# Kernel tuning notes

Hardware: AMD Instinct MI355X
Metric: run time of the kernel (lower is better)

The kernel has to match this reference:

```python
import jax, jax.numpy as jnp
import numpy as np

# --- static config (mirrors init_kwargs) ---
D_MODEL = 512; N_HEADS = 8; E_LAYERS = 2
GLOBAL_TOPK = 32; DOWN_LAYERS = 3; LAYER_NUM = 1
NB = DOWN_LAYERS - LAYER_NUM + 1           # local_band_count = 3
LOCAL_TOPK = GLOBAL_TOPK // NB + 1         # 11
TOPK = GLOBAL_TOPK + NB * LOCAL_TOPK       # all_topk = 65
B, C, L = 16, 32, D_MODEL
LN_EPS = 1e-5


def _layernorm(x, g, b):
    mu = jnp.mean(x, -1, keepdims=True)
    var = jnp.mean((x - mu) ** 2, -1, keepdims=True)
    return (x - mu) / jnp.sqrt(var + LN_EPS) * g + b


def _sigmoid_real(a, b):
    # Re( 1 / (1 + exp(-(a+ib))) )  -- real part of complex sigmoid (torch .float() drops imag)
    ea = jnp.exp(-a)
    wr = 1.0 + ea * jnp.cos(b)
    wi = -ea * jnp.sin(b)
    return wr / (wr * wr + wi * wi)


def _key_freq_indices(mag):
    # cumulative_energy_dynamic: global + per-band top-k on the (B,C)-summed energy
    gm = jnp.sum(mag ** 2, axis=(0, 1))              # [L]
    order = jnp.argsort(-gm)
    idx = [order[:GLOBAL_TOPK]]
    band = L // NB
    for bidx in range(NB):
        s = bidx * band
        e = (bidx + 1) * band if bidx != NB - 1 else L
        idx.append(jnp.argsort(-gm[s:e])[:LOCAL_TOPK] + s)
    return jnp.concatenate(idx)                       # [TOPK]


def _prob_distance(amp, ph, A, w_a, w_p):
    # amp/ph: [B,C,T] -> p: [B,T,T]
    ad = amp[..., :, None] - amp[..., None, :]        # [B,C,T,T]
    pd = ph[..., :, None] - ph[..., None, :]
    fused = w_a * ad + w_p * pd
    temp = jnp.diagonal(A) * fused                    # einsum('dd,bxcd->bxcd')
    dist = jnp.sum(temp * temp, axis=1)               # sum over channel axis -> [B,T,T]
    exp_dist = 1.0 / (dist + 1e-10)
    eye = jnp.eye(TOPK, dtype=exp_dist.dtype)
    offdiag = 1.0 - eye
    exp_dist = exp_dist * offdiag
    exp_max = jax.lax.stop_gradient(jnp.max(exp_dist, -1, keepdims=True))
    p = exp_dist / exp_max
    return (p * offdiag + eye) * 0.99


def _gumbel_mask(p, noise):
    # Bernoulli straight-through gumbel-softmax (tau=1, hard=True)
    flat = p.reshape(-1, 1)
    logit = jnp.log(flat / (1.0 - flat))
    logits = jnp.concatenate([logit, -logit], -1)     # [N,2]
    y = jax.nn.softmax(logits + noise, axis=-1)
    hard = jax.nn.one_hot(jnp.argmax(y, -1), 2, dtype=y.dtype)
    y = hard + y - jax.lax.stop_gradient(y)
    sample = y[..., 0].reshape(B, TOPK, TOPK)
    return jnp.mean(sample, axis=0)                   # [T,T]


def _attention(x, mask, Wq, bq, Wk, bk, Wv, bv, Wo, bo):
    Bn, Lq, D = x.shape
    dh = D // N_HEADS
    q = (x @ Wq.T + bq).reshape(Bn, Lq, N_HEADS, dh)
    k = (x @ Wk.T + bk).reshape(Bn, Lq, N_HEADS, dh)
    v = (x @ Wv.T + bv).reshape(Bn, Lq, N_HEADS, dh)
    scores = jnp.einsum('blhe,bshe->bhls', q, k)
    m = mask[None, None]                              # [1,1,T,T] relation mask
    scores = scores * m + (1.0 - m) * (-1e9)
    attn = jax.nn.softmax(scores / jnp.sqrt(jnp.float32(dh)), -1)
    o = jnp.einsum('bhls,bshd->blhd', attn, v).reshape(Bn, Lq, D)
    return o @ Wo.T + bo


def _forward(x_real, x_imag, gumbel_noise, A, w_amplitude, w_phase,
             Wq, bq, Wk, bk, Wv, bv, Wo, bo, Wc1, bc1, Wc2, bc2,
             g1, b1, g2, b2, gf, bf):
    mag = jnp.sqrt(x_real ** 2 + x_imag ** 2)         # torch.abs of complex x
    ph = jnp.arctan2(x_imag, x_real)                  # torch.angle
    idx = _key_freq_indices(mag)
    key_mag = jnp.take(mag, idx, axis=-1)             # [B,C,T]
    key_ph = jnp.take(ph, idx, axis=-1)
    mask = _gumbel_mask(_prob_distance(key_mag, key_ph, A, w_amplitude, w_phase), gumbel_noise)
    # construct_key_freq_relationship: the magnitude normalizations are identity
    # (mean over a size-1 dim divided by its own sum == 1), so freq/key_freq pass through.
    kr = key_mag * jnp.cos(key_ph)
    ki = key_mag * jnp.sin(key_ph)
    a = kr[..., None] * x_real[:, :, None, :] - ki[..., None] * x_imag[:, :, None, :]
    bI = kr[..., None] * x_imag[:, :, None, :] + ki[..., None] * x_real[:, :, None, :]
    rel = _sigmoid_real(a, bI).astype(jnp.float32)    # [B,C,T,L]
    h = rel.reshape(B * C, TOPK, D_MODEL)
    for l in range(E_LAYERS):
        new_x = _attention(h, mask, Wq[l], bq[l], Wk[l], bk[l], Wv[l], bv[l], Wo[l], bo[l])
        h = _layernorm(h + new_x, g1[l], b1[l])
        y = jax.nn.gelu(h @ Wc1[l].T + bc1[l], approximate=False)
        y = y @ Wc2[l].T + bc2[l]
        h = _layernorm(h + y, g2[l], b2[l])
    h = _layernorm(h, gf, bf)
    full = h.reshape(B, C, TOPK, D_MODEL)
    w = jax.nn.softmax(key_mag, -1)[..., None]        # [B,C,T,1]
    fs = jnp.sum(full * w, axis=2)                    # [B,C,D]
    # torch.polar(full_spectrum, freq_phase) -> return real/imag stacked on last axis
    return jnp.stack([fs * jnp.cos(ph), fs * jnp.sin(ph)], axis=-1)  # [B,C,L,2]


def setup_inputs():
    key = jax.random.key(0)
    ks = jax.random.split(key, 30)
    s = 0.02
    d = D_MODEL
    inp = {
        'x_real': jax.random.normal(ks[0], (B, C, L), jnp.float32),
        'x_imag': jax.random.normal(ks[1], (B, C, L), jnp.float32),
        'gumbel_noise': jax.random.gumbel(ks[2], (B * TOPK * TOPK, 2), jnp.float32),
        'A': jax.random.normal(ks[3], (TOPK, TOPK), jnp.float32),
        'w_amplitude': jnp.array(0.5, jnp.float32),
        'w_phase': jnp.array(0.5, jnp.float32),
        'Wq': jax.random.normal(ks[4], (E_LAYERS, d, d), jnp.float32) * s,
        'bq': jnp.zeros((E_LAYERS, d), jnp.float32),
        'Wk': jax.random.normal(ks[5], (E_LAYERS, d, d), jnp.float32) * s,
        'bk': jnp.zeros((E_LAYERS, d), jnp.float32),
        'Wv': jax.random.normal(ks[6], (E_LAYERS, d, d), jnp.float32) * s,
        'bv': jnp.zeros((E_LAYERS, d), jnp.float32),
        'Wo': jax.random.normal(ks[7], (E_LAYERS, d, d), jnp.float32) * s,
        'bo': jnp.zeros((E_LAYERS, d), jnp.float32),
        'Wc1': jax.random.normal(ks[8], (E_LAYERS, d, d), jnp.float32) * s,
        'bc1': jnp.zeros((E_LAYERS, d), jnp.float32),
        'Wc2': jax.random.normal(ks[9], (E_LAYERS, d, d), jnp.float32) * s,
        'bc2': jnp.zeros((E_LAYERS, d), jnp.float32),
        'g1': jnp.ones((E_LAYERS, d), jnp.float32),
        'b1': jnp.zeros((E_LAYERS, d), jnp.float32),
        'g2': jnp.ones((E_LAYERS, d), jnp.float32),
        'b2': jnp.zeros((E_LAYERS, d), jnp.float32),
        'gf': jnp.ones((d,), jnp.float32),
        'bf': jnp.zeros((d,), jnp.float32),
    }
    return inp


def reference(x_real, x_imag, gumbel_noise, A, w_amplitude, w_phase,
              Wq, bq, Wk, bk, Wv, bv, Wo, bo, Wc1, bc1, Wc2, bc2,
              g1, b1, g2, b2, gf, bf):
    return _forward(x_real, x_imag, gumbel_noise, A, w_amplitude, w_phase,
                    Wq, bq, Wk, bk, Wv, bv, Wo, bo, Wc1, bc1, Wc2, bc2,
                    g1, b1, g2, b2, gf, bf)
```

## Files before the change

kernel.cpp:

```cpp
#include <hip/hip_runtime.h>
#include <hip/hip_bf16.h>

#define BDIM 16
#define CDIM 32
#define LDIM 512
#define TDIM 65
#define DDIM 512
#define BC   (BDIM*CDIM)
#define MROWS (BC*TDIM)
#define LN_EPS 1e-5f

typedef float fx4 __attribute__((ext_vector_type(4)));
typedef __bf16 bf16x8 __attribute__((ext_vector_type(8)));
typedef unsigned short us16;
typedef unsigned short us16x8 __attribute__((ext_vector_type(8)));

__device__ __forceinline__ us16 f2bf(float f){
  unsigned int u = __float_as_uint(f);
  u = (u + 0x7fffu + ((u >> 16) & 1u)) >> 16;
  return (us16)u;
}
__device__ __forceinline__ float bf2f(us16 s){
  return __uint_as_float(((unsigned int)s) << 16);
}
__device__ __forceinline__ float wred_max(float v){
  #pragma unroll
  for (int o = 32; o; o >>= 1) v = fmaxf(v, __shfl_xor(v, o));
  return v;
}
__device__ __forceinline__ float wred_sum(float v){
  #pragma unroll
  for (int o = 32; o; o >>= 1) v += __shfl_xor(v, o);
  return v;
}
__device__ __forceinline__ float gelu_exact(float x){
  return 0.5f * x * (1.0f + erff(x * 0.70710678118654752440f));
}
__device__ __forceinline__ void async16(void* lds, const void* g){
  __builtin_amdgcn_global_load_lds(
      (const __attribute__((address_space(1))) unsigned int*)g,
      (__attribute__((address_space(3))) unsigned int*)lds, 16, 0, 0);
}

__global__ __launch_bounds__(256) void magph_kernel(
    const float* __restrict__ xr, const float* __restrict__ xi,
    float* __restrict__ mag, float* __restrict__ ph)
{
  int i = blockIdx.x * 256 + threadIdx.x;
  float r = xr[i], im = xi[i];
  mag[i] = sqrtf(r*r + im*im);
  ph[i]  = atan2f(im, r);
}

__global__ __launch_bounds__(64) void gm_kernel(
    const float* __restrict__ mag, double* __restrict__ gm)
{
  int l = blockIdx.x, t = threadIdx.x;
  double acc = 0.0;
  #pragma unroll
  for (int r = 0; r < 8; ++r){
    float v = mag[(size_t)(t + 64*r)*LDIM + l];
    acc += (double)v * (double)v;
  }
  #pragma unroll
  for (int o = 32; o; o >>= 1) acc += __shfl_xor(acc, o);
  if (t == 0) gm[l] = acc;
}

__device__ int wave_argmax(const float* val, int lo, int hi, int t){
  float bv = -3.4e38f; int bi = 0x7fffffff;
  for (int i = lo + t; i < hi; i += 64){
    float v = val[i];
    if (v > bv || (v == bv && i < bi)){ bv = v; bi = i; }
  }
  #pragma unroll
  for (int o = 32; o; o >>= 1){
    float ov = __shfl_xor(bv, o); int oi = __shfl_xor(bi, o);
    if (ov > bv || (ov == bv && oi < bi)){ bv = ov; bi = oi; }
  }
  return bi;
}

__global__ __launch_bounds__(64) void topk_kernel(
    const double* __restrict__ gm, int* __restrict__ idxo)
{
  __shared__ float val[LDIM];
  __shared__ float orig[LDIM];
  int t = threadIdx.x;
  for (int i = t; i < LDIM; i += 64){ float v = (float)gm[i]; val[i] = v; orig[i] = v; }
  __syncthreads();
  for (int s = 0; s < 32; ++s){
    int b = wave_argmax(val, 0, LDIM, t);
    if (t == 0){ idxo[s] = b; val[b] = -3.4e38f; }
    __syncthreads();
  }
  for (int i = t; i < LDIM; i += 64) val[i] = orig[i];
  __syncthreads();
  for (int bb = 0; bb < 3; ++bb){
    int s0 = bb*170, e0 = (bb == 2) ? LDIM : (bb+1)*170;
    for (int s = 0; s < 11; ++s){
      int b = wave_argmax(val, s0, e0, t);
      if (t == 0){ idxo[32 + bb*11 + s] = b; val[b] = -3.4e38f; }
      __syncthreads();
    }
  }
}

__global__ __launch_bounds__(64) void keygather_kernel(
    const float* __restrict__ mag, const float* __restrict__ ph, const int* __restrict__ idx,
    float* __restrict__ km, float* __restrict__ kp,
    float* __restrict__ kr, float* __restrict__ ki, float* __restrict__ wsm)
{
  int bc = blockIdx.x, t = threadIdx.x;
  int i0 = idx[t];
  int i1 = idx[64];
  float m0 = mag[(size_t)bc*LDIM + i0];
  float p0 = ph [(size_t)bc*LDIM + i0];
  float m1 = mag[(size_t)bc*LDIM + i1];
  float p1 = ph [(size_t)bc*LDIM + i1];
  size_t o = (size_t)bc*TDIM;
  km[o + t] = m0; kp[o + t] = p0;
  kr[o + t] = m0 * cosf(p0); ki[o + t] = m0 * sinf(p0);
  if (t == 0){
    km[o+64] = m1; kp[o+64] = p1;
    kr[o+64] = m1*cosf(p1); ki[o+64] = m1*sinf(p1);
  }
  float mx = wred_max(fmaxf(m0, m1));
  float e0 = expf(m0 - mx), e1 = expf(m1 - mx);
  float sum = wred_sum(e0) + e1;
  wsm[o + t] = e0 / sum;
  if (t == 0) wsm[o + 64] = e1 / sum;
}

__global__ __launch_bounds__(64) void distmask_kernel(
    const float* __restrict__ km, const float* __restrict__ kp,
    const float* __restrict__ A, const float* __restrict__ wAs, const float* __restrict__ wPs,
    const float* __restrict__ noise, float* __restrict__ mask)
{
  int b = blockIdx.x / TDIM, i = blockIdx.x % TDIM;
  int l = threadIdx.x;
  __shared__ float kmi[CDIM], kpi[CDIM];
  if (l < CDIM){
    kmi[l] = km[(size_t)(b*CDIM + l)*TDIM + i];
    kpi[l] = kp[(size_t)(b*CDIM + l)*TDIM + i];
  }
  __syncthreads();
  float wa = wAs[0], wp = wPs[0];
  float ed0, ed1 = 0.f;
  {
    int j = l;
    float Ad = A[j*TDIM + j];
    float acc = 0.f;
    for (int c = 0; c < CDIM; ++c){
      float d = Ad * (wa*(kmi[c] - km[(size_t)(b*CDIM+c)*TDIM + j])
                    + wp*(kpi[c] - kp[(size_t)(b*CDIM+c)*TDIM + j]));
      acc += d*d;
    }
    ed0 = (j == i) ? 0.f : 1.0f/(acc + 1e-10f);
  }
  if (l == 0){
    int j = 64;
    float Ad = A[j*TDIM + j];
    float acc = 0.f;
    for (int c = 0; c < CDIM; ++c){
      float d = Ad * (wa*(kmi[c] - km[(size_t)(b*CDIM+c)*TDIM + j])
                    + wp*(kpi[c] - kp[(size_t)(b*CDIM+c)*TDIM + j]));
      acc += d*d;
    }
    ed1 = (j == i) ? 0.f : 1.0f/(acc + 1e-10f);
  }
  float mx = ed0;
  if (l == 0) mx = fmaxf(mx, ed1);
  mx = wred_max(mx);
  {
    int j = l;
    float pv = (j == i) ? 0.99f : 0.99f * (ed0 / mx);
    float logit = logf(pv / (1.0f - pv));
    size_t n = ((size_t)b*TDIM + i)*TDIM + j;
    float g0 = noise[2*n], g1 = noise[2*n + 1];
    if (logit + g0 >= g1 - logit) atomicAdd(&mask[i*TDIM + j], 0.0625f);
  }
  if (l == 0){
    int j = 64;
    float pv = (j == i) ? 0.99f : 0.99f * (ed1 / mx);
    float logit = logf(pv / (1.0f - pv));
    size_t n = ((size_t)b*TDIM + i)*TDIM + j;
    float g0 = noise[2*n], g1 = noise[2*n + 1];
    if (logit + g0 >= g1 - logit) atomicAdd(&mask[i*TDIM + j], 0.0625f);
  }
}

__global__ __launch_bounds__(256) void rel_kernel(
    const float* __restrict__ xr, const float* __restrict__ xi,
    const float* __restrict__ kr, const float* __restrict__ ki,
    us16* __restrict__ hb)
{
  size_t e = (size_t)blockIdx.x * 256 + threadIdx.x;
  int d = (int)(e & 511);
  size_t mt = e >> 9;
  int t  = (int)(mt % TDIM);
  int bc = (int)(mt / TDIM);
  float krv = kr[(size_t)bc*TDIM + t], kiv = ki[(size_t)bc*TDIM + t];
  float r = xr[(size_t)bc*LDIM + d], im = xi[(size_t)bc*LDIM + d];
  float a  = krv*r - kiv*im;
  float bb = krv*im + kiv*r;
  float ea = expf(-a);
  float sn, cs; sincosf(bb, &sn, &cs);
  float wr = 1.0f + ea*cs;
  float wi = -ea*sn;
  float rel = wr / (wr*wr + wi*wi);
  hb[e] = f2bf(rel);
}

__global__ __launch_bounds__(256) void convert_kernel(
    const float* __restrict__ s, us16* __restrict__ d, int n)
{
  int i = blockIdx.x * 256 + threadIdx.x;
  if (i < n) d[i] = f2bf(s[i]);
}

template<int EPI>
__global__ __launch_bounds__(256) void gemm_bt(
    const us16* __restrict__ X, const us16* __restrict__ W,
    const float* __restrict__ bias, us16* __restrict__ outB)
{
  __shared__ us16 As[128*32];
  __shared__ us16 Bs[128*32];
  const int tid = threadIdx.x;
  const int w = tid >> 6, l = tid & 63;
  const int m0 = blockIdx.x * 128, n0 = blockIdx.y * 128;
  const int wm = w >> 1, wn = w & 1;
  const int g = l >> 4, li = l & 15;
  fx4 acc[4][4] = {};

  for (int k0 = 0; k0 < 512; k0 += 32){
    #pragma unroll
    for (int q = 0; q < 2; ++q){
      int c = w*128 + q*64 + l;
      int row = c >> 2, slot = c & 3;
      int koct = (slot ^ (row & 3)) << 3;
      const us16* srcA = X + (size_t)(m0 + row)*512 + k0 + koct;
      const us16* srcB = W + (size_t)(n0 + row)*512 + k0 + koct;
      async16(&As[(w*128 + q*64)*8], srcA);
      async16(&Bs[(w*128 + q*64)*8], srcB);
    }
    __syncthreads();
    bf16x8 aF[4], bF[4];
    #pragma unroll
    for (int mi = 0; mi < 4; ++mi){
      int r = wm*64 + mi*16 + li;
      int chunk = 4*r + (g ^ (r & 3));
      aF[mi] = *reinterpret_cast<const bf16x8*>(&As[chunk*8]);
    }
    #pragma unroll
    for (int ni = 0; ni < 4; ++ni){
      int cn = wn*64 + ni*16 + li;
      int chunk = 4*cn + (g ^ (cn & 3));
      bF[ni] = *reinterpret_cast<const bf16x8*>(&Bs[chunk*8]);
    }
    #pragma unroll
    for (int mi = 0; mi < 4; ++mi)
      #pragma unroll
      for (int ni = 0; ni < 4; ++ni)
        acc[mi][ni] = __builtin_amdgcn_mfma_f32_16x16x32_bf16(aF[mi], bF[ni], acc[mi][ni], 0, 0, 0);
    __syncthreads();
  }

  #pragma unroll
  for (int mi = 0; mi < 4; ++mi){
    #pragma unroll
    for (int ni = 0; ni < 4; ++ni){
      int col = n0 + wn*64 + ni*16 + li;
      float bv = bias[col];
      #pragma unroll
      for (int r = 0; r < 4; ++r){
        int row = m0 + wm*64 + mi*16 + g*4 + r;
        float v = acc[mi][ni][r] + bv;
        if (EPI == 2) v = gelu_exact(v);
        outB[(size_t)row*512 + col] = f2bf(v);
      }
    }
  }
}

__global__ __launch_bounds__(256) void attn_mfma(
    const us16* __restrict__ qb, const us16* __restrict__ kb, const us16* __restrict__ vb,
    const float* __restrict__ mask, us16* __restrict__ ob)
{
  __shared__ __align__(16) us16 Qs[80*64];
  __shared__ __align__(16) us16 Ks[80*64];
  __shared__ __align__(16) us16 Vt[64*96];
  __shared__ __align__(16) us16 Pb[80*96];
  const int bn = blockIdx.x, h = blockIdx.y;
  const int tid = threadIdx.x;
  const int w = tid >> 6, l = tid & 63;
  const int g = l >> 4, li = l & 15;
  const size_t gbase = ((size_t)bn*TDIM)*512 + h*64;

  {
    uint2 z = {0u, 0u};
    for (int u = tid; u < 1536; u += 256) ((uint2*)Vt)[u] = z;
    for (int u = tid; u < 1920; u += 256) ((uint2*)Pb)[u] = z;
  }
  #pragma unroll
  for (int it = 0; it < 2; ++it){
    int u = it*256 + tid;
    int r = u >> 3, ps = u & 7;
    int slog = ps ^ (r & 7);
    async16(&Qs[(it*256 + w*64)*8], qb + gbase + (size_t)r*512 + slog*8);
    async16(&Ks[(it*256 + w*64)*8], kb + gbase + (size_t)r*512 + slog*8);
  }
  us16 vreg[17];
  #pragma unroll
  for (int i = 0; i < 17; ++i){
    int k = i*4 + w;
    if (k <= 64) vreg[i] = vb[gbase + (size_t)k*512 + l];
  }
  uint4 r64 = {};
  if (tid < 8)       r64 = *(const uint4*)(qb + gbase + (size_t)64*512 + tid*8);
  else if (tid < 16) r64 = *(const uint4*)(kb + gbase + (size_t)64*512 + (tid-8)*8);

  __syncthreads();

  if (tid < 8)       *(uint4*)&Qs[(64*8 + tid)*8] = r64;
  else if (tid < 16) *(uint4*)&Ks[(64*8 + (tid-8))*8] = r64;
  #pragma unroll
  for (int i = 0; i < 17; ++i){
    int k = i*4 + w;
    if (k <= 64){
      int d = l, s = k >> 3;
      int ps = (s < 8) ? (s ^ (d & 7)) : (8 + ((s & 3) ^ (d & 3)));
      Vt[d*96 + ps*8 + (k & 7)] = vreg[i];
    }
  }
  __syncthreads();

  for (int m = w; m < 5; m += 4){
    const int mbase = m*16;
    fx4 acc[5] = {};
    #pragma unroll
    for (int kk = 0; kk < 2; ++kk){
      int ra = mbase + li;
      int sA = (kk*4 + g) ^ (ra & 7);
      bf16x8 aF = *(const bf16x8*)&Qs[ra*64 + sA*8];
      #pragma unroll
      for (int n = 0; n < 5; ++n){
        int rb = n*16 + li;
        int sB = (kk*4 + g) ^ (rb & 7);
        bf16x8 bF = *(const bf16x8*)&Ks[rb*64 + sB*8];
        acc[n] = __builtin_amdgcn_mfma_f32_16x16x32_bf16(aF, bF, acc[n], 0, 0, 0);
      }
    }
    float p[5][4];
    #pragma unroll
    for (int reg = 0; reg < 4; ++reg){
      int i = mbase + g*4 + reg;
      float sv[5], mx = -3.4e38f;
      #pragma unroll
      for (int n = 0; n < 5; ++n){
        int j = n*16 + li;
        if (j < TDIM){
          float mv = (i < TDIM) ? mask[i*TDIM + j] : 0.0f;
          sv[n] = (acc[n][reg]*mv + (1.0f - mv)*(-1e9f)) * 0.125f;
        } else sv[n] = -3.4e38f;
        mx = fmaxf(mx, sv[n]);
      }
      #pragma unroll
      for (int o = 1; o < 16; o <<= 1) mx = fmaxf(mx, __shfl_xor(mx, o));
      float sum = 0.f;
      #pragma unroll
      for (int n = 0; n < 5; ++n){
        int j = n*16 + li;
        float e = (j < TDIM) ? expf(sv[n] - mx) : 0.0f;
        p[n][reg] = e; sum += e;
      }
      #pragma unroll
      for (int o = 1; o < 16; o <<= 1) sum += __shfl_xor(sum, o);
      float inv = 1.0f / sum;
      #pragma unroll
      for (int n = 0; n < 5; ++n) p[n][reg] *= inv;
    }
    #pragma unroll
    for (int n = 0; n < 5; ++n){
      int j = n*16 + li, s = j >> 3, jo = j & 7;
      #pragma unroll
      for (int reg = 0; reg < 4; ++reg){
        int r = mbase + g*4 + reg;
        int ps = (s < 8) ? (s ^ (r & 7)) : (8 + ((s & 3) ^ (r & 3)));
        Pb[r*96 + ps*8 + jo] = f2bf(p[n][reg]);
      }
    }
    asm volatile("s_waitcnt lgkmcnt(0)" ::: "memory");
    fx4 acc2[4] = {};
    #pragma unroll
    for (int kk = 0; kk < 3; ++kk){
      int ra = mbase + li;
      int s = kk*4 + g;
      int psA = (s < 8) ? (s ^ (ra & 7)) : (8 + ((s & 3) ^ (ra & 3)));
      bf16x8 pF = *(const bf16x8*)&Pb[ra*96 + psA*8];
      #pragma unroll
      for (int n2 = 0; n2 < 4; ++n2){
        int d = n2*16 + li;
        int psB = (s < 8) ? (s ^ (d & 7)) : (8 + ((s & 3) ^ (d & 3)));
        bf16x8 vF = *(const bf16x8*)&Vt[d*96 + psB*8];
        acc2[n2] = __builtin_amdgcn_mfma_f32_16x16x32_bf16(pF, vF, acc2[n2], 0, 0, 0);
      }
    }
    #pragma unroll
    for (int n2 = 0; n2 < 4; ++n2){
      int d = n2*16 + li;
      #pragma unroll
      for (int reg = 0; reg < 4; ++reg){
        int i = mbase + g*4 + reg;
        if (i < TDIM) ob[gbase + (size_t)i*512 + d] = f2bf(acc2[n2][reg]);
      }
    }
  }
}

__global__ __launch_bounds__(256) void ln_kernel(
    const us16* __restrict__ X, const us16* __restrict__ R,
    const float* __restrict__ g, const float* __restrict__ b,
    us16* __restrict__ out)
{
  int row = blockIdx.x*4 + (threadIdx.x >> 6);
  int l = threadIdx.x & 63;
  size_t base = (size_t)row*DDIM + l*8;
  us16x8 xv = *(const us16x8*)(X + base);
  float v[8];
  #pragma unroll
  for (int e = 0; e < 8; ++e) v[e] = bf2f(xv[e]);
  if (R){
    us16x8 rv = *(const us16x8*)(R + base);
    #pragma unroll
    for (int e = 0; e < 8; ++e) v[e] += bf2f(rv[e]);
  }
  float s = 0.f;
  #pragma unroll
  for (int e = 0; e < 8; ++e) s += v[e];
  float mu = wred_sum(s) * (1.0f/512.0f);
  float qq = 0.f;
  #pragma unroll
  for (int e = 0; e < 8; ++e){ float d = v[e] - mu; qq += d*d; }
  float var = wred_sum(qq) * (1.0f/512.0f);
  float inv = 1.0f / sqrtf(var + LN_EPS);
  fx4 g0 = *(const fx4*)&g[l*8], g1 = *(const fx4*)&g[l*8 + 4];
  fx4 b0 = *(const fx4*)&b[l*8], b1 = *(const fx4*)&b[l*8 + 4];
  us16x8 o;
  #pragma unroll
  for (int e = 0; e < 4; ++e){
    o[e]     = f2bf((v[e]   - mu) * inv * g0[e] + b0[e]);
    o[e + 4] = f2bf((v[e+4] - mu) * inv * g1[e] + b1[e]);
  }
  *(us16x8*)(out + base) = o;
}

__global__ __launch_bounds__(512) void final_kernel(
    const us16* __restrict__ hfin, const float* __restrict__ wsm,
    const float* __restrict__ ph, float* __restrict__ out)
{
  int bc = blockIdx.x, d = threadIdx.x;
  __shared__ float wv[TDIM];
  if (d < TDIM) wv[d] = wsm[(size_t)bc*TDIM + d];
  __syncthreads();
  float fs = 0.f;
  for (int t = 0; t < TDIM; ++t)
    fs += bf2f(hfin[((size_t)bc*TDIM + t)*DDIM + d]) * wv[t];
  float p = ph[(size_t)bc*LDIM + d];
  float sn, cs; sincosf(p, &sn, &cs);
  out[((size_t)bc*LDIM + d)*2 + 0] = fs * cs;
  out[((size_t)bc*LDIM + d)*2 + 1] = fs * sn;
}

extern "C" void kernel_launch(void* const* d_in, const int* in_sizes, int n_in,
                              void* d_out, int out_size, void* d_ws, size_t ws_size,
                              hipStream_t stream)
{
  const float* xr    = (const float*)d_in[0];
  const float* xi    = (const float*)d_in[1];
  const float* noise = (const float*)d_in[2];
  const float* Amat  = (const float*)d_in[3];
  const float* wA    = (const float*)d_in[4];
  const float* wP    = (const float*)d_in[5];
  const float* Wq    = (const float*)d_in[6];
  const float* bq    = (const float*)d_in[7];
  const float* Wk    = (const float*)d_in[8];
  const float* bk    = (const float*)d_in[9];
  const float* Wv    = (const float*)d_in[10];
  const float* bv    = (const float*)d_in[11];
  const float* Wo    = (const float*)d_in[12];
  const float* bo    = (const float*)d_in[13];
  const float* Wc1   = (const float*)d_in[14];
  const float* bc1   = (const float*)d_in[15];
  const float* Wc2   = (const float*)d_in[16];
  const float* bc2   = (const float*)d_in[17];
  const float* g1    = (const float*)d_in[18];
  const float* b1    = (const float*)d_in[19];
  const float* g2    = (const float*)d_in[20];
  const float* b2    = (const float*)d_in[21];
  const float* gf    = (const float*)d_in[22];
  const float* bfin  = (const float*)d_in[23];
  float* out = (float*)d_out;

  char* p = (char*)d_ws;
  auto take = [&](size_t bytes) -> char* {
    char* r = p; p += (bytes + 255) & ~(size_t)255; return r;
  };
  float*  mag  = (float*)take((size_t)BC*LDIM*4);
  float*  ph   = (float*)take((size_t)BC*LDIM*4);
  double* gm   = (double*)take(LDIM*8);
  int*    idx  = (int*)take(TDIM*4);
  float*  km   = (float*)take((size_t)BC*TDIM*4);
  float*  kp   = (float*)take((size_t)BC*TDIM*4);
  float*  kr   = (float*)take((size_t)BC*TDIM*4);
  float*  ki   = (float*)take((size_t)BC*TDIM*4);
  float*  wsm  = (float*)take((size_t)BC*TDIM*4);
  float*  mask = (float*)take(TDIM*TDIM*4);
  us16*   wbf  = (us16*)take((size_t)6*2*DDIM*DDIM*2);
  us16*   hb   = (us16*)take((size_t)MROWS*DDIM*2);
  us16*   qb   = (us16*)take((size_t)MROWS*DDIM*2);
  us16*   kb2  = (us16*)take((size_t)MROWS*DDIM*2);
  us16*   vb2  = (us16*)take((size_t)MROWS*DDIM*2);
  us16*   ob   = (us16*)take((size_t)MROWS*DDIM*2);
  us16*   t0b  = vb2;
  us16*   yb   = qb;

  magph_kernel<<<dim3(1024), dim3(256), 0, stream>>>(xr, xi, mag, ph);
  gm_kernel<<<dim3(LDIM), dim3(64), 0, stream>>>(mag, gm);
  topk_kernel<<<dim3(1), dim3(64), 0, stream>>>(gm, idx);
  keygather_kernel<<<dim3(BC), dim3(64), 0, stream>>>(mag, ph, idx, km, kp, kr, ki, wsm);
  hipMemsetAsync(mask, 0, TDIM*TDIM*4, stream);
  distmask_kernel<<<dim3(BDIM*TDIM), dim3(64), 0, stream>>>(km, kp, Amat, wA, wP, noise, mask);
  rel_kernel<<<dim3(66560), dim3(256), 0, stream>>>(xr, xi, kr, ki, hb);

  const float* Wsrc[6] = {Wq, Wk, Wv, Wo, Wc1, Wc2};
  for (int m = 0; m < 6; ++m)
    convert_kernel<<<dim3(2048), dim3(256), 0, stream>>>(
        Wsrc[m], wbf + (size_t)m*2*DDIM*DDIM, 2*DDIM*DDIM);

  dim3 ggrid(MROWS/128, DDIM/128);
  for (int l = 0; l < 2; ++l){
    const us16* wq_  = wbf + ((size_t)0*2 + l)*DDIM*DDIM;
    const us16* wk_  = wbf + ((size_t)1*2 + l)*DDIM*DDIM;
    const us16* wv_  = wbf + ((size_t)2*2 + l)*DDIM*DDIM;
    const us16* wo_  = wbf + ((size_t)3*2 + l)*DDIM*DDIM;
    const us16* wc1_ = wbf + ((size_t)4*2 + l)*DDIM*DDIM;
    const us16* wc2_ = wbf + ((size_t)5*2 + l)*DDIM*DDIM;

    gemm_bt<0><<<ggrid, 256, 0, stream>>>(hb, wq_, bq + (size_t)l*DDIM, qb);
    gemm_bt<0><<<ggrid, 256, 0, stream>>>(hb, wk_, bk + (size_t)l*DDIM, kb2);
    gemm_bt<0><<<ggrid, 256, 0, stream>>>(hb, wv_, bv + (size_t)l*DDIM, vb2);
    attn_mfma<<<dim3(BC, 8), dim3(256), 0, stream>>>(qb, kb2, vb2, mask, ob);
    gemm_bt<0><<<ggrid, 256, 0, stream>>>(ob, wo_, bo + (size_t)l*DDIM, t0b);
    ln_kernel<<<dim3(MROWS/4), dim3(256), 0, stream>>>(t0b, hb, g1 + (size_t)l*DDIM, b1 + (size_t)l*DDIM, hb);
    gemm_bt<2><<<ggrid, 256, 0, stream>>>(hb, wc1_, bc1 + (size_t)l*DDIM, yb);
    gemm_bt<0><<<ggrid, 256, 0, stream>>>(yb, wc2_, bc2 + (size_t)l*DDIM, t0b);
    ln_kernel<<<dim3(MROWS/4), dim3(256), 0, stream>>>(t0b, hb, g2 + (size_t)l*DDIM, b2 + (size_t)l*DDIM, hb);
  }
  ln_kernel<<<dim3(MROWS/4), dim3(256), 0, stream>>>(hb, nullptr, gf, bfin, t0b);
  final_kernel<<<dim3(BC), dim3(512), 0, stream>>>(t0b, wsm, ph, out);
}
```

Baseline: 874.9 us.

## Fuse QKV GEMMs, widen GEMM K-tile, rank-based topk, batch weight conversion

Merges the three Q/K/V projections into one GEMM over a concatenated 1536-column weight, with outputs routed by column block. The GEMM K-tile grows from 32 to 64 with an 8-way swizzle, so there are half as many barriers per tile. The serial 64-thread argmax top-k becomes a parallel rank computation over 512 threads. Six weight-conversion launches become one that also packs the QKV biases. The attention kernel now loads V with vectorized transposed stores and zeroes only the padding slots, at the cost of more shared memory per GEMM block and more complex indexing.

New measurement: 821.2 us. -6.1%, faster.

```diff
diff --git a/kernel.cpp b/kernel.cpp
--- a/kernel.cpp
+++ b/kernel.cpp
@@ -67,43 +67,29 @@
   if (t == 0) gm[l] = acc;
 }
 
-__device__ int wave_argmax(const float* val, int lo, int hi, int t){
-  float bv = -3.4e38f; int bi = 0x7fffffff;
-  for (int i = lo + t; i < hi; i += 64){
-    float v = val[i];
-    if (v > bv || (v == bv && i < bi)){ bv = v; bi = i; }
-  }
-  #pragma unroll
-  for (int o = 32; o; o >>= 1){
-    float ov = __shfl_xor(bv, o); int oi = __shfl_xor(bi, o);
-    if (ov > bv || (ov == bv && oi < bi)){ bv = ov; bi = oi; }
-  }
-  return bi;
-}
-
-__global__ __launch_bounds__(64) void topk_kernel(
+__global__ __launch_bounds__(256) void topk_kernel(
     const double* __restrict__ gm, int* __restrict__ idxo)
 {
   __shared__ float val[LDIM];
-  __shared__ float orig[LDIM];
   int t = threadIdx.x;
-  for (int i = t; i < LDIM; i += 64){ float v = (float)gm[i]; val[i] = v; orig[i] = v; }
+  int i = blockIdx.x * 256 + t;
+  val[t] = (float)gm[t];
+  val[t + 256] = (float)gm[t + 256];
   __syncthreads();
-  for (int s = 0; s < 32; ++s){
-    int b = wave_argmax(val, 0, LDIM, t);
-    if (t == 0){ idxo[s] = b; val[b] = -3.4e38f; }
-    __syncthreads();
-  }
-  for (int i = t; i < LDIM; i += 64) val[i] = orig[i];
-  __syncthreads();
-  for (int bb = 0; bb < 3; ++bb){
-    int s0 = bb*170, e0 = (bb == 2) ? LDIM : (bb+1)*170;
-    for (int s = 0; s < 11; ++s){
-      int b = wave_argmax(val, s0, e0, t);
-      if (t == 0){ idxo[32 + bb*11 + s] = b; val[b] = -3.4e38f; }
-      __syncthreads();
-    }
-  }
+  float vi = val[i];
+  int band = (i < 170) ? 0 : (i < 340 ? 1 : 2);
+  int lo = band * 170;
+  int hi = (band == 2) ? LDIM : lo + 170;
+  int gr = 0, br = 0;
+  #pragma unroll 4
+  for (int o = 0; o < LDIM; ++o){
+    float vo = val[o];
+    bool ahead = (vo > vi) || (vo == vi && o < i);
+    gr += ahead ? 1 : 0;
+    br += (ahead && o >= lo && o < hi) ? 1 : 0;
+  }
+  if (gr < 32) idxo[gr] = i;
+  if (br < 11) idxo[32 + band*11 + br] = i;
 }
 
 __global__ __launch_bounds__(64) void keygather_kernel(
@@ -212,20 +198,39 @@
   hb[e] = f2bf(rel);
 }
 
-__global__ __launch_bounds__(256) void convert_kernel(
-    const float* __restrict__ s, us16* __restrict__ d, int n)
-{
-  int i = blockIdx.x * 256 + threadIdx.x;
-  if (i < n) d[i] = f2bf(s[i]);
+struct WPtrs { const float* s[6]; };
+__global__ __launch_bounds__(256) void convert_all(
+    WPtrs wp, const float* __restrict__ bq, const float* __restrict__ bk,
+    const float* __restrict__ bv,
+    us16* __restrict__ wqkv, us16* __restrict__ wo,
+    us16* __restrict__ wc1, us16* __restrict__ wc2, float* __restrict__ bqkv)
+{
+  size_t i = (size_t)blockIdx.x * 256 + threadIdx.x;
+  int m   = (int)(i >> 19);
+  int rem = (int)(i & 524287);
+  int l   = rem >> 18;
+  us16 b = f2bf(wp.s[m][rem]);
+  if (m < 3)      wqkv[(size_t)l*786432 + m*262144 + (rem & 262143)] = b;
+  else if (m == 3) wo[rem]  = b;
+  else if (m == 4) wc1[rem] = b;
+  else             wc2[rem] = b;
+  if (i < 3072){
+    int l2 = (int)(i >> 11);
+    int n  = (int)(i & 1535);
+    int mm = n >> 9, c = n & 511;
+    const float* bs = (mm == 0) ? bq : ((mm == 1) ? bk : bv);
+    bqkv[i] = bs[l2*512 + c];
+  }
 }
 
 template<int EPI>
 __global__ __launch_bounds__(256) void gemm_bt(
     const us16* __restrict__ X, const us16* __restrict__ W,
-    const float* __restrict__ bias, us16* __restrict__ outB)
-{
-  __shared__ us16 As[128*32];
-  __shared__ us16 Bs[128*32];
+    const float* __restrict__ bias,
+    us16* __restrict__ o0, us16* __restrict__ o1, us16* __restrict__ o2)
+{
+  __shared__ us16 As[128*64];
+  __shared__ us16 Bs[128*64];
   const int tid = threadIdx.x;
   const int w = tid >> 6, l = tid & 63;
   const int m0 = blockIdx.x * 128, n0 = blockIdx.y * 128;
@@ -233,51 +238,55 @@
   const int g = l >> 4, li = l & 15;
   fx4 acc[4][4] = {};
 
-  for (int k0 = 0; k0 < 512; k0 += 32){
-    #pragma unroll
-    for (int q = 0; q < 2; ++q){
-      int c = w*128 + q*64 + l;
-      int row = c >> 2, slot = c & 3;
-      int koct = (slot ^ (row & 3)) << 3;
-      const us16* srcA = X + (size_t)(m0 + row)*512 + k0 + koct;
-      const us16* srcB = W + (size_t)(n0 + row)*512 + k0 + koct;
-      async16(&As[(w*128 + q*64)*8], srcA);
-      async16(&Bs[(w*128 + q*64)*8], srcB);
+  for (int k0 = 0; k0 < 512; k0 += 64){
+    #pragma unroll
+    for (int q = 0; q < 4; ++q){
+      int c = q*256 + tid;
+      int row = c >> 3, ps = c & 7;
+      int sl = ps ^ (row & 7);
+      async16(&As[c*8], X + (size_t)(m0 + row)*512 + k0 + sl*8);
+      async16(&Bs[c*8], W + (size_t)(n0 + row)*512 + k0 + sl*8);
     }
     __syncthreads();
-    bf16x8 aF[4], bF[4];
-    #pragma unroll
-    for (int mi = 0; mi < 4; ++mi){
-      int r = wm*64 + mi*16 + li;
-      int chunk = 4*r + (g ^ (r & 3));
-      aF[mi] = *reinterpret_cast<const bf16x8*>(&As[chunk*8]);
-    }
+    #pragma unroll
+    for (int kk = 0; kk < 2; ++kk){
+      bf16x8 aF[4], bF[4];
+      #pragma unroll
+      for (int mi = 0; mi < 4; ++mi){
+        int r = wm*64 + mi*16 + li;
+        int s = (kk*4 + g) ^ (r & 7);
+        aF[mi] = *reinterpret_cast<const bf16x8*>(&As[(r*8 + s)*8]);
+      }
+      #pragma unroll
+      for (int ni = 0; ni < 4; ++ni){
+        int rn = wn*64 + ni*16 + li;
+        int s = (kk*4 + g) ^ (rn & 7);
+        bF[ni] = *reinterpret_cast<const bf16x8*>(&Bs[(rn*8 + s)*8]);
+      }
+      #pragma unroll
+      for (int mi = 0; mi < 4; ++mi)
+        #pragma unroll
+        for (int ni = 0; ni < 4; ++ni)
+          acc[mi][ni] = __builtin_amdgcn_mfma_f32_16x16x32_bf16(aF[mi], bF[ni], acc[mi][ni], 0, 0, 0);
+    }
+    __syncthreads();
+  }
+
+  const int sel = n0 >> 9;
+  us16* dst = (sel == 0) ? o0 : ((sel == 1) ? o1 : o2);
+  #pragma unroll
+  for (int mi = 0; mi < 4; ++mi){
     #pragma unroll
     for (int ni = 0; ni < 4; ++ni){
-      int cn = wn*64 + ni*16 + li;
-      int chunk = 4*cn + (g ^ (cn & 3));
-      bF[ni] = *reinterpret_cast<const bf16x8*>(&Bs[chunk*8]);
-    }
-    #pragma unroll
-    for (int mi = 0; mi < 4; ++mi)
-      #pragma unroll
-      for (int ni = 0; ni < 4; ++ni)
-        acc[mi][ni] = __builtin_amdgcn_mfma_f32_16x16x32_bf16(aF[mi], bF[ni], acc[mi][ni], 0, 0, 0);
-    __syncthreads();
-  }
-
-  #pragma unroll
-  for (int mi = 0; mi < 4; ++mi){
-    #pragma unroll
-    for (int ni = 0; ni < 4; ++ni){
-      int col = n0 + wn*64 + ni*16 + li;
-      float bv = bias[col];
+      int coln = wn*64 + ni*16 + li;
+      float bv = bias[n0 + coln];
+      int col = (n0 & 511) + coln;
       #pragma unroll
       for (int r = 0; r < 4; ++r){
         int row = m0 + wm*64 + mi*16 + g*4 + r;
         float v = acc[mi][ni][r] + bv;
         if (EPI == 2) v = gelu_exact(v);
-        outB[(size_t)row*512 + col] = f2bf(v);
+        dst[(size_t)row*512 + col] = f2bf(v);
       }
     }
   }
@@ -298,9 +307,9 @@
   const size_t gbase = ((size_t)bn*TDIM)*512 + h*64;
 
   {
-    uint2 z = {0u, 0u};
-    for (int u = tid; u < 1536; u += 256) ((uint2*)Vt)[u] = z;
-    for (int u = tid; u < 1920; u += 256) ((uint2*)Pb)[u] = z;
+    uint4 z = {0u,0u,0u,0u};
+    if (tid < 160){ int r = tid >> 1, sl = 10 + (tid & 1); *(uint4*)&Pb[r*96 + sl*8] = z; }
+    if (tid < 192){ int r = tid & 63, sl = 9 + (tid >> 6); *(uint4*)&Vt[r*96 + sl*8] = z; }
   }
   #pragma unroll
   for (int it = 0; it < 2; ++it){
@@ -310,12 +319,12 @@
     async16(&Qs[(it*256 + w*64)*8], qb + gbase + (size_t)r*512 + slog*8);
     async16(&Ks[(it*256 + w*64)*8], kb + gbase + (size_t)r*512 + slog*8);
   }
-  us16 vreg[17];
-  #pragma unroll
-  for (int i = 0; i < 17; ++i){
-    int k = i*4 + w;
-    if (k <= 64) vreg[i] = vb[gbase + (size_t)k*512 + l];
-  }
+  us16 vreg[16];
+  #pragma unroll
+  for (int j = 0; j < 16; ++j)
+    vreg[j] = vb[gbase + (size_t)(w*16 + j)*512 + l];
+  us16 v64v = 0;
+  if (tid < 64) v64v = vb[gbase + (size_t)64*512 + tid];
   uint4 r64 = {};
   if (tid < 8)       r64 = *(const uint4*)(qb + gbase + (size_t)64*512 + tid*8);
   else if (tid < 16) r64 = *(const uint4*)(kb + gbase + (size_t)64*512 + (tid-8)*8);
@@ -324,14 +333,18 @@
 
   if (tid < 8)       *(uint4*)&Qs[(64*8 + tid)*8] = r64;
   else if (tid < 16) *(uint4*)&Ks[(64*8 + (tid-8))*8] = r64;
-  #pragma unroll
-  for (int i = 0; i < 17; ++i){
-    int k = i*4 + w;
-    if (k <= 64){
-      int d = l, s = k >> 3;
-      int ps = (s < 8) ? (s ^ (d & 7)) : (8 + ((s & 3) ^ (d & 3)));
-      Vt[d*96 + ps*8 + (k & 7)] = vreg[i];
-    }
+  {
+    us16x8 lo, hi;
+    #pragma unroll
+    for (int j = 0; j < 8; ++j){ lo[j] = vreg[j]; hi[j] = vreg[8+j]; }
+    int s0 = w*2, s1 = w*2 + 1;
+    *(us16x8*)&Vt[l*96 + (s0 ^ (l & 7))*8] = lo;
+    *(us16x8*)&Vt[l*96 + (s1 ^ (l & 7))*8] = hi;
+  }
+  if (tid < 64){
+    us16x8 t8 = {};
+    t8[0] = v64v;
+    *(us16x8*)&Vt[tid*96 + 8*8] = t8;
   }
   __syncthreads();
 
@@ -386,7 +399,7 @@
       #pragma unroll
       for (int reg = 0; reg < 4; ++reg){
         int r = mbase + g*4 + reg;
-        int ps = (s < 8) ? (s ^ (r & 7)) : (8 + ((s & 3) ^ (r & 3)));
+        int ps = (s < 8) ? (s ^ (r & 7)) : s;
         Pb[r*96 + ps*8 + jo] = f2bf(p[n][reg]);
       }
     }
@@ -396,12 +409,12 @@
     for (int kk = 0; kk < 3; ++kk){
       int ra = mbase + li;
       int s = kk*4 + g;
-      int psA = (s < 8) ? (s ^ (ra & 7)) : (8 + ((s & 3) ^ (ra & 3)));
+      int psA = (s < 8) ? (s ^ (ra & 7)) : s;
       bf16x8 pF = *(const bf16x8*)&Pb[ra*96 + psA*8];
       #pragma unroll
       for (int n2 = 0; n2 < 4; ++n2){
         int d = n2*16 + li;
-        int psB = (s < 8) ? (s ^ (d & 7)) : (8 + ((s & 3) ^ (d & 3)));
+        int psB = (s < 8) ? (s ^ (d & 7)) : s;
         bf16x8 vF = *(const bf16x8*)&Vt[d*96 + psB*8];
         acc2[n2] = __builtin_amdgcn_mfma_f32_16x16x32_bf16(pF, vF, acc2[n2], 0, 0, 0);
       }
@@ -516,7 +529,11 @@
   float*  ki   = (float*)take((size_t)BC*TDIM*4);
   float*  wsm  = (float*)take((size_t)BC*TDIM*4);
   float*  mask = (float*)take(TDIM*TDIM*4);
-  us16*   wbf  = (us16*)take((size_t)6*2*DDIM*DDIM*2);
+  us16*   wqkv = (us16*)take((size_t)2*1536*512*2);
+  us16*   wo3  = (us16*)take((size_t)2*512*512*2);
+  us16*   wc13 = (us16*)take((size_t)2*512*512*2);
+  us16*   wc23 = (us16*)take((size_t)2*512*512*2);
+  float*  bqkv = (float*)take((size_t)2*1536*4);
   us16*   hb   = (us16*)take((size_t)MROWS*DDIM*2);
   us16*   qb   = (us16*)take((size_t)MROWS*DDIM*2);
   us16*   kb2  = (us16*)take((size_t)MROWS*DDIM*2);
@@ -527,34 +544,24 @@
 
   magph_kernel<<<dim3(1024), dim3(256), 0, stream>>>(xr, xi, mag, ph);
   gm_kernel<<<dim3(LDIM), dim3(64), 0, stream>>>(mag, gm);
-  topk_kernel<<<dim3(1), dim3(64), 0, stream>>>(gm, idx);
+  topk_kernel<<<dim3(2), dim3(256), 0, stream>>>(gm, idx);
   keygather_kernel<<<dim3(BC), dim3(64), 0, stream>>>(mag, ph, idx, km, kp, kr, ki, wsm);
   hipMemsetAsync(mask, 0, TDIM*TDIM*4, stream);
   distmask_kernel<<<dim3(BDIM*TDIM), dim3(64), 0, stream>>>(km, kp, Amat, wA, wP, noise, mask);
   rel_kernel<<<dim3(66560), dim3(256), 0, stream>>>(xr, xi, kr, ki, hb);
 
-  const float* Wsrc[6] = {Wq, Wk, Wv, Wo, Wc1, Wc2};
-  for (int m = 0; m < 6; ++m)
-    convert_kernel<<<dim3(2048), dim3(256), 0, stream>>>(
-        Wsrc[m], wbf + (size_t)m*2*DDIM*DDIM, 2*DDIM*DDIM);
-
-  dim3 ggrid(MROWS/128, DDIM/128);
+  WPtrs wp; wp.s[0]=Wq; wp.s[1]=Wk; wp.s[2]=Wv; wp.s[3]=Wo; wp.s[4]=Wc1; wp.s[5]=Wc2;
+  convert_all<<<dim3(12288), dim3(256), 0, stream>>>(wp, bq, bk, bv, wqkv, wo3, wc13, wc23, bqkv);
+
+  dim3 gqkv(MROWS/128, 1536/128);
+  dim3 g512(MROWS/128, 512/128);
   for (int l = 0; l < 2; ++l){
-    const us16* wq_  = wbf + ((size_t)0*2 + l)*DDIM*DDIM;
-    const us16* wk_  = wbf + ((size_t)1*2 + l)*DDIM*DDIM;
-    const us16* wv_  = wbf + ((size_t)2*2 + l)*DDIM*DDIM;
-    const us16* wo_  = wbf + ((size_t)3*2 + l)*DDIM*DDIM;
-    const us16* wc1_ = wbf + ((size_t)4*2 + l)*DDIM*DDIM;
-    const us16* wc2_ = wbf + ((size_t)5*2 + l)*DDIM*DDIM;
-
-    gemm_bt<0><<<ggrid, 256, 0, stream>>>(hb, wq_, bq + (size_t)l*DDIM, qb);
-    gemm_bt<0><<<ggrid, 256, 0, stream>>>(hb, wk_, bk + (size_t)l*DDIM, kb2);
-    gemm_bt<0><<<ggrid, 256, 0, stream>>>(hb, wv_, bv + (size_t)l*DDIM, vb2);
+    gemm_bt<0><<<gqkv, 256, 0, stream>>>(hb, wqkv + (size_t)l*786432, bqkv + (size_t)l*1536, qb, kb2, vb2);
     attn_mfma<<<dim3(BC, 8), dim3(256), 0, stream>>>(qb, kb2, vb2, mask, ob);
-    gemm_bt<0><<<ggrid, 256, 0, stream>>>(ob, wo_, bo + (size_t)l*DDIM, t0b);
+    gemm_bt<0><<<g512, 256, 0, stream>>>(ob, wo3 + (size_t)l*262144, bo + (size_t)l*DDIM, t0b, t0b, t0b);
     ln_kernel<<<dim3(MROWS/4), dim3(256), 0, stream>>>(t0b, hb, g1 + (size_t)l*DDIM, b1 + (size_t)l*DDIM, hb);
-    gemm_bt<2><<<ggrid, 256, 0, stream>>>(hb, wc1_, bc1 + (size_t)l*DDIM, yb);
-    gemm_bt<0><<<ggrid, 256, 0, stream>>>(yb, wc2_, bc2 + (size_t)l*DDIM, t0b);
+    gemm_bt<2><<<g512, 256, 0, stream>>>(hb, wc13 + (size_t)l*262144, bc1 + (size_t)l*DDIM, yb, yb, yb);
+    gemm_bt<0><<<g512, 256, 0, stream>>>(yb, wc23 + (size_t)l*262144, bc2 + (size_t)l*DDIM, t0b, t0b, t0b);
     ln_kernel<<<dim3(MROWS/4), dim3(256), 0, stream>>>(t0b, hb, g2 + (size_t)l*DDIM, b2 + (size_t)l*DDIM, hb);
   }
   ln_kernel<<<dim3(MROWS/4), dim3(256), 0, stream>>>(hb, nullptr, gf, bfin, t0b);
```
